# Kernel tuning notes

Hardware: AMD Instinct MI355X
Metric: run time of the kernel (lower is better)

## Reference

```python
import jax, jax.numpy as jnp
import numpy as np

N_NODES = 50000
N_EDGES = 400000
D_NODE = 256
D_EDGE = 64
HEADS = 32          # node_hidden_size // 8
HEAD_DIM = 8        # node_hidden_size // heads
LRELU = 0.01


def _lin_init(key, fan_in, fan_out, bias=True):
    kw, kb = jax.random.split(key)
    s = 1.0 / np.sqrt(fan_in)
    W = jax.random.uniform(kw, (fan_in, fan_out), jnp.float32, -s, s)
    if bias:
        b = jax.random.uniform(kb, (fan_out,), jnp.float32, -s, s)
        return W, b
    return W


def setup_inputs() -> dict:
    key = jax.random.key(0)
    ks = jax.random.split(key, 12)
    x = jax.random.normal(ks[0], (N_NODES, D_NODE), jnp.float32)
    edge_index = jax.random.randint(ks[1], (2, N_EDGES), 0, N_NODES, jnp.int64)
    edge_attr = jax.random.normal(ks[2], (N_EDGES, D_EDGE), jnp.float32)
    Wq, bq = _lin_init(ks[3], D_NODE, D_NODE)
    Wk, bk = _lin_init(ks[4], D_NODE, D_NODE)
    Wv, bv = _lin_init(ks[5], D_NODE, D_NODE)
    We = _lin_init(ks[6], D_EDGE, D_NODE, bias=False)   # lin_edge has no bias in PyG
    Ws, bs = _lin_init(ks[7], D_NODE, D_NODE)           # root/skip connection
    W1, b1 = _lin_init(ks[8], 2 * D_NODE + D_EDGE, D_EDGE)
    W2, b2 = _lin_init(ks[9], D_EDGE, D_EDGE)
    return dict(x=x, edge_index=edge_index, edge_attr=edge_attr,
                Wq=Wq, bq=bq, Wk=Wk, bk=bk, Wv=Wv, bv=bv, We=We,
                Ws=Ws, bs=bs, W1=W1, b1=b1, W2=W2, b2=b2)


def _leaky(v, alpha=LRELU):
    return jnp.where(v >= 0, v, alpha * v)


def reference(x, edge_index, edge_attr, Wq, bq, Wk, bk, Wv, bv, We, Ws, bs, W1, b1, W2, b2):
    N = x.shape[0]
    src, dst = edge_index[0], edge_index[1]

    # ---- TransformerConv (concat heads, root weight, edge_dim) ----
    q = (x @ Wq + bq).reshape(N, HEADS, HEAD_DIM)
    k = (x @ Wk + bk).reshape(N, HEADS, HEAD_DIM)
    v = (x @ Wv + bv).reshape(N, HEADS, HEAD_DIM)
    e = (edge_attr @ We).reshape(-1, HEADS, HEAD_DIM)           # [E,H,C]

    k_j = k[src] + e                                            # [E,H,C]
    alpha = jnp.einsum('ehc,ehc->eh', q[dst], k_j) / np.sqrt(HEAD_DIM)
    # segment softmax over destination nodes
    amax = jax.ops.segment_max(alpha, dst, num_segments=N)      # [N,H]
    ex = jnp.exp(alpha - amax[dst])
    denom = jax.ops.segment_sum(ex, dst, num_segments=N)        # [N,H]
    attn = ex / (denom[dst] + 1e-16)                            # [E,H]

    msg = (v[src] + e) * attn[:, :, None]                       # [E,H,C]
    out = jax.ops.segment_sum(msg, dst, num_segments=N).reshape(N, D_NODE)
    out = out + (x @ Ws + bs)                                   # skip / root weight

    x_new = _leaky(out)                                         # block activation

    # ---- EdgeResidualLayer ----
    h = jnp.concatenate([x_new[src], x_new[dst], edge_attr], axis=-1)  # [E,576]
    h = _leaky(h @ W1 + b1)
    edge_new = edge_attr + (h @ W2 + b2)
    edge_new = _leaky(edge_new)

    return (x_new, edge_new)
```

## Files before the change

### kernel.cpp

```cpp
#include <hip/hip_runtime.h>
#include <hip/hip_bf16.h>


#define N_NODES 50000
#define N_EDGES 400000
#define D_NODE 256
#define D_EDGE 64
#define HEADS 32
#define LRELU 0.01f
#define SEG 16

typedef __hip_bfloat16 bf16;
typedef __attribute__((ext_vector_type(8))) short short8b;
typedef __attribute__((ext_vector_type(4))) float f32x4;
typedef __attribute__((ext_vector_type(4))) unsigned short ushort4v;
typedef __attribute__((ext_vector_type(4))) int int4v;

__device__ __forceinline__ float bf2f(bf16 v) { return __bfloat162float(v); }
__device__ __forceinline__ bf16 f2bf(float f) { return __float2bfloat16(f); }
__device__ __forceinline__ float bfraw(unsigned short u) {
    return __uint_as_float(((unsigned int)u) << 16);
}
__device__ __forceinline__ unsigned short rawbf(float f) {
    bf16 t = f2bf(f); return *(unsigned short*)&t;
}
__device__ __forceinline__ float leaky(float v) { return v >= 0.f ? v : LRELU * v; }
__device__ __forceinline__ short8b pack8(const f32x4 a, const f32x4 b) {
    short8b r;
    r[0] = (short)rawbf(a[0]); r[1] = (short)rawbf(a[1]);
    r[2] = (short)rawbf(a[2]); r[3] = (short)rawbf(a[3]);
    r[4] = (short)rawbf(b[0]); r[5] = (short)rawbf(b[1]);
    r[6] = (short)rawbf(b[2]); r[7] = (short)rawbf(b[3]);
    return r;
}

__global__ void k0_detect(const int* __restrict__ ei, int* __restrict__ flags)
{
    const int lane = threadIdx.x;
    const unsigned long long mz = __ballot(ei[2 * lane + 1] == 0);
    if (lane == 0) flags[0] = (__popcll(mz) >= 48) ? 1 : 0;
}

__device__ __forceinline__ void load_edge(const int* ei, int f, int i, int& s, int& d)
{
    if (f) {
        const long long* e64 = (const long long*)ei;
        s = (int)e64[i]; d = (int)e64[N_EDGES + i];
    } else {
        s = ei[i]; d = ei[N_EDGES + i];
    }
}

__global__ __launch_bounds__(256) void kcd_degree(
    const int* __restrict__ ei, const int* __restrict__ flags, int* __restrict__ deg)
{
    const int i = blockIdx.x * 256 + threadIdx.x;
    if (i >= N_EDGES) return;
    int s, d; load_edge(ei, flags[0], i, s, d);
    atomicAdd(&deg[d], 1);
}

__global__ __launch_bounds__(1024) void kcs_scan(int* __restrict__ cur)
{
    __shared__ int ps[1024];
    const int t = threadIdx.x;
    const int CHN = (N_NODES + 1023) / 1024;
    const int base = t * CHN;
    int sum = 0;
    for (int i = 0; i < CHN; ++i) {
        const int n = base + i;
        if (n < N_NODES) sum += cur[n];
    }
    ps[t] = sum;
    __syncthreads();
    for (int off = 1; off < 1024; off <<= 1) {
        const int v = (t >= off) ? ps[t - off] : 0;
        __syncthreads();
        ps[t] += v;
        __syncthreads();
    }
    int excl = (t == 0) ? 0 : ps[t - 1];
    for (int i = 0; i < CHN; ++i) {
        const int n = base + i;
        if (n < N_NODES) {
            const int d = cur[n];
            cur[n] = excl;
            excl += d;
        }
    }
}

__global__ __launch_bounds__(256) void kct_scatter(
    const int* __restrict__ ei, const int* __restrict__ flags, int* __restrict__ cursor,
    int* __restrict__ ssort, int* __restrict__ dsort, int* __restrict__ eidsort)
{
    const int i = blockIdx.x * 256 + threadIdx.x;
    if (i >= N_EDGES) return;
    int s, d; load_edge(ei, flags[0], i, s, d);
    const int pos = atomicAdd(&cursor[d], 1);
    ssort[pos] = s; dsort[pos] = d; eidsort[pos] = i;
}

__global__ __launch_bounds__(256) void kT_transpose(
    const float* __restrict__ We, const float* __restrict__ W1, const float* __restrict__ W2,
    const float* __restrict__ Wq, const float* __restrict__ Wk,
    const float* __restrict__ Wv, const float* __restrict__ Ws,
    bf16* __restrict__ WeTf, bf16* __restrict__ W1sdf, bf16* __restrict__ W1eaf,
    bf16* __restrict__ W2Tf, bf16* __restrict__ WT4f)
{
    const int gid = blockIdx.x * 256 + threadIdx.x;
    const int gsz = gridDim.x * 256;
    for (int i = gid; i < 4 * 16 * 8 * 512; i += gsz) {
        const int j = i & 7, l = (i >> 3) & 63, kc = (i >> 9) & 7;
        const int ct = (i >> 12) & 15, m = i >> 16;
        const int row = l & 15, kg = l >> 4;
        const int n = ct * 16 + row, k = kc * 32 + kg * 8 + j;
        const float* W = (m == 0) ? Wq : (m == 1) ? Wk : (m == 2) ? Wv : Ws;
        WT4f[i] = f2bf(W[k * 256 + n]);
    }
    for (int i = gid; i < 16 * 2 * 512; i += gsz) {
        const int j = i & 7, l = (i >> 3) & 63, kc = (i >> 9) & 1, ct = i >> 10;
        const int row = l & 15, kg = l >> 4;
        const int n = ct * 16 + row, k = kc * 32 + kg * 8 + j;
        WeTf[i] = f2bf(We[k * 256 + n]);
    }
    for (int i = gid; i < 2 * 4 * 8 * 512; i += gsz) {
        const int j = i & 7, l = (i >> 3) & 63, kc = (i >> 9) & 7;
        const int ct = (i >> 12) & 3, m2 = i >> 14;
        const int row = l & 15, kg = l >> 4;
        const int n = ct * 16 + row;
        const int k = m2 * 256 + kc * 32 + kg * 8 + j;
        W1sdf[i] = f2bf(W1[k * 64 + n]);
    }
    for (int i = gid; i < 4 * 2 * 512; i += gsz) {
        const int j = i & 7, l = (i >> 3) & 63, kc = (i >> 9) & 1, ct = i >> 10;
        const int row = l & 15, kg = l >> 4;
        const int n = ct * 16 + row;
        const int k = 512 + kc * 32 + kg * 8 + j;
        W1eaf[i] = f2bf(W1[k * 64 + n]);
    }
    for (int i = gid; i < 4 * 2 * 512; i += gsz) {
        const int j = i & 7, l = (i >> 3) & 63, kc = (i >> 9) & 1, ct = i >> 10;
        const int row = l & 15, kg = l >> 4;
        const int n = ct * 16 + row, k = kc * 32 + kg * 8 + j;
        W2Tf[i] = f2bf(W2[k * 64 + n]);
    }
}

#define X_LD 264
__global__ __launch_bounds__(256) void k1_node_mfma(
    const float* __restrict__ x, const bf16* __restrict__ WT4f,
    const float* __restrict__ bq, const float* __restrict__ bk,
    const float* __restrict__ bv, const float* __restrict__ bs,
    bf16* __restrict__ qo, bf16* __restrict__ kvb,
    bf16* __restrict__ skipb)
{
    __shared__ unsigned short xs[64 * X_LD];
    const int tid = threadIdx.x;
    const int n0 = blockIdx.x * 64;
    const int w = tid >> 6, l = tid & 63;
    const int row = l & 15, kg = l >> 4;

    {
        const int e = tid >> 2, t = tid & 3;
        const int nmine = n0 + e;
        const f32x4* src = (const f32x4*)(x + (size_t)nmine * 256 + t * 64);
        #pragma unroll
        for (int c = 0; c < 4; ++c) {
            unsigned short tmp[16];
            if (nmine < N_NODES) {
                #pragma unroll
                for (int u = 0; u < 4; ++u) {
                    const f32x4 v = __builtin_nontemporal_load(src + c * 4 + u);
                    tmp[u * 4 + 0] = rawbf(v[0]); tmp[u * 4 + 1] = rawbf(v[1]);
                    tmp[u * 4 + 2] = rawbf(v[2]); tmp[u * 4 + 3] = rawbf(v[3]);
                }
            } else {
                #pragma unroll
                for (int u = 0; u < 16; ++u) tmp[u] = 0;
            }
            *(short8b*)&xs[e * X_LD + t * 64 + c * 16]     = *(short8b*)&tmp[0];
            *(short8b*)&xs[e * X_LD + t * 64 + c * 16 + 8] = *(short8b*)&tmp[8];
        }
    }
    short8b af[8];
    #pragma unroll
    for (int kc = 0; kc < 8; ++kc)
        af[kc] = *(const short8b*)&xs[(w * 16 + row) * X_LD + kc * 32 + kg * 8];

    for (int m = 0; m < 4; ++m) {
        const float* bias = (m == 0) ? bq : (m == 1) ? bk : (m == 2) ? bv : bs;
        #pragma unroll 4
        for (int ct = 0; ct < 16; ++ct) {
            const float bvv = bias[ct * 16 + row];
            f32x4 acc = {bvv, bvv, bvv, bvv};
            #pragma unroll
            for (int kc = 0; kc < 8; ++kc) {
                const short8b bfr = *(const short8b*)(WT4f + (((size_t)((m * 16 + ct) * 8 + kc)) << 9) + l * 8);
                acc = __builtin_amdgcn_mfma_f32_16x16x32_bf16(af[kc], bfr, acc, 0, 0, 0);
            }
            #pragma unroll
            for (int r = 0; r < 4; ++r)
                xs[(w * 16 + kg * 4 + r) * X_LD + ct * 16 + row] = rawbf(acc[r]);
        }
        {
            #pragma unroll
            for (int u = 0; u < 8; ++u) {
                const int flat = u * 64 + l;
                const int node = w * 16 + (flat >> 5);
                const int col8 = (flat & 31) * 8;
                if (n0 + node < N_NODES) {
                    const short8b vdat = *(const short8b*)&xs[node * X_LD + col8];
                    bf16* dp;
                    if (m == 0)      dp = qo    + (size_t)(n0 + node) * 256 + col8;
                    else if (m == 1) dp = kvb   + (size_t)(n0 + node) * 512 + col8;
                    else if (m == 2) dp = kvb   + (size_t)(n0 + node) * 512 + 256 + col8;
                    else             dp = skipb + (size_t)(n0 + node) * 256 + col8;
                    *(short8b*)dp = vdat;
                }
            }
        }
    }
}

#define EP_LD 264
__global__ __launch_bounds__(256) void k2_seg(
    const int* __restrict__ ssort, const int* __restrict__ dsort,
    const int* __restrict__ eidsort, const int* __restrict__ endptr,
    const float* __restrict__ ea, const bf16* __restrict__ WeTf,
    const bf16* __restrict__ q, const bf16* __restrict__ kvb,
    const bf16* __restrict__ skipb, const bf16* __restrict__ W1sdf,
    float* __restrict__ out_x, bf16* __restrict__ xnb, bf16* __restrict__ P)
{
    __shared__ float acc_s[SEG * 256];
    __shared__ float den_s[SEG * HEADS];
    __shared__ unsigned short ep_s[64 * EP_LD];
    const int tid = threadIdx.x;
    const int n0 = blockIdx.x * SEG;

    #pragma unroll
    for (int i = 0; i < SEG; ++i) acc_s[i * 256 + tid] = 0.f;
    if (tid < SEG * HEADS - 256) den_s[256 + tid] = 0.f;
    den_s[tid] = 0.f;

    const int start = (n0 == 0) ? 0 : endptr[n0 - 1];
    const int end   = endptr[n0 + SEG - 1];
    __syncthreads();

    const int w = tid >> 6, l = tid & 63;
    const int row = l & 15, kg = l >> 4;
    const float scale = 0.35355339059327373f;

    for (int sbase = start + w * 16; sbase < end; sbase += 64) {
        const int cnt = min(16, end - sbase);

        short8b af0 = {0, 0, 0, 0, 0, 0, 0, 0}, af1 = af0;
        if (row < cnt) {
            const int eg = eidsort[sbase + row];
            const float* pb = ea + (size_t)eg * 64 + kg * 8;
            const f32x4 a0 = __builtin_nontemporal_load((const f32x4*)pb);
            const f32x4 a1 = __builtin_nontemporal_load((const f32x4*)(pb + 4));
            const f32x4 b0 = __builtin_nontemporal_load((const f32x4*)(pb + 32));
            const f32x4 b1 = __builtin_nontemporal_load((const f32x4*)(pb + 36));
            af0 = pack8(a0, a1); af1 = pack8(b0, b1);
        }

        int sv = 0;
        if (l < 16)      { if (l < cnt)      sv = ssort[sbase + l]; }
        else if (l < 32) { if (l - 16 < cnt) sv = dsort[sbase + (l - 16)]; }

        ushort4v kvv[16], vvv[16];
        #pragma unroll
        for (int i = 0; i < 16; ++i) {
            const int s = __shfl(sv, min(i, cnt - 1));
            const bf16* base = kvb + (size_t)s * 512;
            kvv[i] = *(const ushort4v*)(base + l * 4);
            vvv[i] = *(const ushort4v*)(base + 256 + l * 4);
        }
        __builtin_amdgcn_sched_barrier(0);

        #pragma unroll 4
        for (int ct = 0; ct < 16; ++ct) {
            f32x4 acc = {0.f, 0.f, 0.f, 0.f};
            const short8b b0 = *(const short8b*)(WeTf + (ct * 2 + 0) * 512 + l * 8);
            const short8b b1 = *(const short8b*)(WeTf + (ct * 2 + 1) * 512 + l * 8);
            acc = __builtin_amdgcn_mfma_f32_16x16x32_bf16(af0, b0, acc, 0, 0, 0);
            acc = __builtin_amdgcn_mfma_f32_16x16x32_bf16(af1, b1, acc, 0, 0, 0);
            #pragma unroll
            for (int r = 0; r < 4; ++r)
                ep_s[(w * 16 + kg * 4 + r) * EP_LD + ct * 16 + row] = rawbf(acc[r]);
        }

        float macc[4] = {0.f, 0.f, 0.f, 0.f};
        float dacc = 0.f;
        int dprev = -1;
        ushort4v qv = {0, 0, 0, 0};

        #pragma unroll
        for (int i = 0; i < 16; ++i) {
            const int d = __shfl(sv, 16 + min(i, cnt - 1));
            if (d != dprev) {
                if (dprev >= 0) {
                    const int ld = dprev - n0;
                    #pragma unroll
                    for (int t = 0; t < 4; ++t)
                        atomicAdd(&acc_s[ld * 256 + l * 4 + t], macc[t]);
                    if ((l & 1) == 0)
                        atomicAdd(&den_s[ld * HEADS + (l >> 1)], dacc);
                    macc[0] = macc[1] = macc[2] = macc[3] = 0.f;
                    dacc = 0.f;
                }
                qv = *(const ushort4v*)(q + (size_t)d * 256 + l * 4);
                dprev = d;
            }
            const ushort4v ep = *(const ushort4v*)&ep_s[(w * 16 + i) * EP_LD + l * 4];
            float p = 0.f, m4[4];
            #pragma unroll
            for (int t = 0; t < 4; ++t) {
                const float epf = bfraw(ep[t]);
                p = fmaf(bfraw(qv[t]), bfraw(kvv[i][t]) + epf, p);
                m4[t] = bfraw(vvv[i][t]) + epf;
            }
            p += __shfl_xor(p, 1);
            const float ex = (i < cnt) ? __expf(p * scale) : 0.f;
            #pragma unroll
            for (int t = 0; t < 4; ++t) macc[t] = fmaf(m4[t], ex, macc[t]);
            dacc += ex;
        }
        {
            const int ld = dprev - n0;
            #pragma unroll
            for (int t = 0; t < 4; ++t)
                atomicAdd(&acc_s[ld * 256 + l * 4 + t], macc[t]);
            if ((l & 1) == 0)
                atomicAdd(&den_s[ld * HEADS + (l >> 1)], dacc);
        }
    }
    __syncthreads();

    #pragma unroll
    for (int u = 0; u < 4; ++u) {
        const int flat4 = u * 256 + tid;
        const int node = flat4 >> 6;
        const int ch4 = flat4 & 63;
        const int n = n0 + node;
        const float den = den_s[node * HEADS + (ch4 >> 1)] + 1e-16f;
        const f32x4 mv = *(const f32x4*)&acc_s[node * 256 + ch4 * 4];
        const ushort4v sk = *(const ushort4v*)(skipb + (size_t)n * 256 + ch4 * 4);
        f32x4 o; ushort4v ob;
        #pragma unroll
        for (int t = 0; t < 4; ++t) {
            const float xn = leaky(mv[t] / den + bfraw(sk[t]));
            o[t] = xn; ob[t] = rawbf(xn);
        }
        *(f32x4*)(out_x + (size_t)n * 256 + ch4 * 4) = o;
        *(ushort4v*)(xnb + (size_t)n * 256 + ch4 * 4) = ob;
        *(ushort4v*)&ep_s[node * EP_LD + ch4 * 4] = ob;
    }
    __syncthreads();

    {
        short8b af2[8];
        #pragma unroll
        for (int kc = 0; kc < 8; ++kc)
            af2[kc] = *(const short8b*)&ep_s[row * EP_LD + kc * 32 + kg * 8];
        #pragma unroll
        for (int c2 = 0; c2 < 2; ++c2) {
            const int ct = w * 2 + c2;
            const int m2 = ct >> 2, ct4 = ct & 3;
            f32x4 acc = {0.f, 0.f, 0.f, 0.f};
            #pragma unroll
            for (int kc = 0; kc < 8; ++kc) {
                const short8b bfr = *(const short8b*)(W1sdf + ((m2 * 4 + ct4) * 8 + kc) * 512 + l * 8);
                acc = __builtin_amdgcn_mfma_f32_16x16x32_bf16(af2[kc], bfr, acc, 0, 0, 0);
            }
            #pragma unroll
            for (int r = 0; r < 4; ++r)
                P[(size_t)(n0 + kg * 4 + r) * 128 + m2 * 64 + row * 4 + ct4] = f2bf(acc[r]);
        }
    }
}

__global__ __launch_bounds__(256) void k4_edge_mlp(
    const int* __restrict__ ssort, const int* __restrict__ dsort,
    const int* __restrict__ eidsort,
    const bf16* __restrict__ P, const float* __restrict__ ea,
    const bf16* __restrict__ W1eaf, const float* __restrict__ b1,
    const bf16* __restrict__ W2Tf, const float* __restrict__ b2,
    float* __restrict__ out_e)
{
    __shared__ unsigned short h2_s[4][16 * 72];
    __shared__ unsigned short ea_s[4][16 * 72];
    const int tid = threadIdx.x;
    const int w = tid >> 6, l = tid & 63;
    const int row = l & 15, kg = l >> 4;

    const int q8 = (N_EDGES / 64) >> 3, r8 = (N_EDGES / 64) & 7;
    const int xcd = blockIdx.x & 7, idx = blockIdx.x >> 3;
    const int bid = (xcd < r8 ? xcd * (q8 + 1) : r8 * (q8 + 1) + (xcd - r8) * q8) + idx;
    const int e0 = bid * 64;
    const int sl = e0 + w * 16 + row;
    const int eg = eidsort[sl];

    const int cr0 = e0 + w * 16 + kg * 4;
    const int4v s4  = *(const int4v*)(ssort + cr0);
    const int4v d4  = *(const int4v*)(dsort + cr0);
    const int4v eg4 = *(const int4v*)(eidsort + cr0);

    const float* pb = ea + (size_t)eg * 64 + kg * 8;
    const f32x4 a0 = __builtin_nontemporal_load((const f32x4*)pb);
    const f32x4 a1 = __builtin_nontemporal_load((const f32x4*)(pb + 4));
    const f32x4 c0 = __builtin_nontemporal_load((const f32x4*)(pb + 32));
    const f32x4 c1 = __builtin_nontemporal_load((const f32x4*)(pb + 36));

    const unsigned short* Pu = (const unsigned short*)P;
    ushort4v ps4[4], pd4[4];
    #pragma unroll
    for (int r = 0; r < 4; ++r) {
        ps4[r] = *(const ushort4v*)(Pu + (size_t)s4[r] * 128 + row * 4);
        pd4[r] = *(const ushort4v*)(Pu + (size_t)d4[r] * 128 + 64 + row * 4);
    }
    __builtin_amdgcn_sched_barrier(0);

    const short8b afr0 = pack8(a0, a1);
    const short8b afr1 = pack8(c0, c1);
    *(short8b*)&ea_s[w][row * 72 + kg * 8]      = afr0;
    *(short8b*)&ea_s[w][row * 72 + 32 + kg * 8] = afr1;

    f32x4 acc[4];
    #pragma unroll
    for (int ct = 0; ct < 4; ++ct) {
        const float bvv = b1[ct * 16 + row];
        acc[ct] = (f32x4){bvv, bvv, bvv, bvv};
    }
    #pragma unroll
    for (int kc = 0; kc < 2; ++kc) {
        const short8b af = (kc == 0) ? afr0 : afr1;
        #pragma unroll
        for (int ct = 0; ct < 4; ++ct) {
            const short8b bfr = *(const short8b*)(W1eaf + (ct * 2 + kc) * 512 + l * 8);
            acc[ct] = __builtin_amdgcn_mfma_f32_16x16x32_bf16(af, bfr, acc[ct], 0, 0, 0);
        }
    }
    #pragma unroll
    for (int ct = 0; ct < 4; ++ct)
        #pragma unroll
        for (int r = 0; r < 4; ++r)
            acc[ct][r] += bfraw(ps4[r][ct]) + bfraw(pd4[r][ct]);

    unsigned short* h2 = h2_s[w];
    #pragma unroll
    for (int ct = 0; ct < 4; ++ct)
        #pragma unroll
        for (int r = 0; r < 4; ++r)
            h2[(kg * 4 + r) * 72 + ct * 16 + row] = rawbf(leaky(acc[ct][r]));

    f32x4 a2[4];
    #pragma unroll
    for (int ct = 0; ct < 4; ++ct) {
        const float bvv = b2[ct * 16 + row];
        a2[ct] = (f32x4){bvv, bvv, bvv, bvv};
    }
    #pragma unroll
    for (int kc = 0; kc < 2; ++kc) {
        const short8b af = *(const short8b*)&h2[row * 72 + kc * 32 + kg * 8];
        #pragma unroll
        for (int ct = 0; ct < 4; ++ct) {
            const short8b bfr = *(const short8b*)(W2Tf + (ct * 2 + kc) * 512 + l * 8);
            a2[ct] = __builtin_amdgcn_mfma_f32_16x16x32_bf16(af, bfr, a2[ct], 0, 0, 0);
        }
    }

    #pragma unroll
    for (int ct = 0; ct < 4; ++ct)
        #pragma unroll
        for (int r = 0; r < 4; ++r) {
            const float eav = bfraw(ea_s[w][(kg * 4 + r) * 72 + ct * 16 + row]);
            out_e[(size_t)eg4[r] * 64 + ct * 16 + row] = leaky(eav + a2[ct][r]);
        }
}

extern "C" void kernel_launch(void* const* d_in, const int* in_sizes, int n_in,
                              void* d_out, int out_size, void* d_ws, size_t ws_size,
                              hipStream_t stream)
{
    const float* x  = (const float*)d_in[0];
    const int*   ei = (const int*)d_in[1];
    const float* ea = (const float*)d_in[2];
    const float* Wq = (const float*)d_in[3];
    const float* bq = (const float*)d_in[4];
    const float* Wk = (const float*)d_in[5];
    const float* bk = (const float*)d_in[6];
    const float* Wv = (const float*)d_in[7];
    const float* bv = (const float*)d_in[8];
    const float* We = (const float*)d_in[9];
    const float* Ws = (const float*)d_in[10];
    const float* bs = (const float*)d_in[11];
    const float* W1 = (const float*)d_in[12];
    const float* b1 = (const float*)d_in[13];
    const float* W2 = (const float*)d_in[14];
    const float* b2 = (const float*)d_in[15];

    char* ws = (char*)d_ws;
    int*   flags  = (int*)ws;
    int*   ssort  = (int*)(ws + 4096);
    int*   dsort  = (int*)(ws + 1604096);
    int*   eids   = (int*)(ws + 3204096);
    int*   cursor = (int*)(ws + 4804096);
    bf16*  WeTf   = (bf16*)(ws + 5004096);
    bf16*  W1sdf  = (bf16*)(ws + 5036864);
    bf16*  W1eaf  = (bf16*)(ws + 5102400);
    bf16*  W2Tf   = (bf16*)(ws + 5110592);
    bf16*  WT4f   = (bf16*)(ws + 5118784);
    bf16*  qb     = (bf16*)(ws + 5643072);
    bf16*  kvb    = (bf16*)(ws + 31243072);
    bf16*  xnb    = (bf16*)(ws + 82443072);
    bf16*  Pp     = (bf16*)(ws + 108100000);

    float* out_x = (float*)d_out;
    float* out_e = out_x + (size_t)N_NODES * D_NODE;
    bf16*  skipb = (bf16*)out_e;

    hipMemsetAsync(cursor, 0, N_NODES * 4, stream);

    k0_detect<<<1, 64, 0, stream>>>(ei, flags);
    kcd_degree<<<(N_EDGES + 255) / 256, 256, 0, stream>>>(ei, flags, cursor);
    kcs_scan<<<1, 1024, 0, stream>>>(cursor);
    kct_scatter<<<(N_EDGES + 255) / 256, 256, 0, stream>>>(ei, flags, cursor, ssort, dsort, eids);

    kT_transpose<<<64, 256, 0, stream>>>(We, W1, W2, Wq, Wk, Wv, Ws,
                                         WeTf, W1sdf, W1eaf, W2Tf, WT4f);

    k1_node_mfma<<<(N_NODES + 63) / 64, 256, 0, stream>>>(
        x, WT4f, bq, bk, bv, bs, qb, kvb, skipb);

    k2_seg<<<N_NODES / SEG, 256, 0, stream>>>(
        ssort, dsort, eids, cursor, ea, WeTf, qb, kvb, skipb, W1sdf,
        out_x, xnb, Pp);

    k4_edge_mlp<<<N_EDGES / 64, 256, 0, stream>>>(
        ssort, dsort, eids, Pp, ea, W1eaf, b1, W2Tf, b2, out_e);
}
```

Before: 561.9 us.

## Pre-permute edge attributes to sorted bf16 buffer and drop unused xnb store

Adds a kernel that gathers edge_attr in destination-sorted order and converts it to a contiguous bf16 buffer. The segment and edge-MLP kernels then read half-size, coalesced rows instead of doing random fp32 gathers through eidsort, and the edge-MLP no longer stages edge attributes in shared memory. The unused bf16 x_new write is also removed. The cost is one extra pass that reads ea (fp32, random) and writes a 51MB bf16 copy, plus an extra launch.

```diff
diff --git a/kernel.cpp b/kernel.cpp
--- a/kernel.cpp
+++ b/kernel.cpp
@@ -99,6 +99,26 @@
     int s, d; load_edge(ei, flags[0], i, s, d);
     const int pos = atomicAdd(&cursor[d], 1);
     ssort[pos] = s; dsort[pos] = d; eidsort[pos] = i;
+}
+
+__global__ __launch_bounds__(256) void keir_reorder(
+    const int* __restrict__ eidsort, const float* __restrict__ ea,
+    bf16* __restrict__ easb)
+{
+    const int tid = threadIdx.x;
+    const int e = blockIdx.x * 64 + (tid >> 2);
+    const int t = tid & 3;
+    const int eg = eidsort[e];
+    const f32x4* src = (const f32x4*)(ea + (size_t)eg * 64 + t * 16);
+    unsigned short tmp[16];
+    #pragma unroll
+    for (int u = 0; u < 4; ++u) {
+        const f32x4 v = __builtin_nontemporal_load(src + u);
+        tmp[u * 4 + 0] = rawbf(v[0]); tmp[u * 4 + 1] = rawbf(v[1]);
+        tmp[u * 4 + 2] = rawbf(v[2]); tmp[u * 4 + 3] = rawbf(v[3]);
+    }
+    *(short8b*)(easb + (size_t)e * 64 + t * 16)     = *(short8b*)&tmp[0];
+    *(short8b*)(easb + (size_t)e * 64 + t * 16 + 8) = *(short8b*)&tmp[8];
 }
 
 __global__ __launch_bounds__(256) void kT_transpose(
@@ -226,11 +246,11 @@
 #define EP_LD 264
 __global__ __launch_bounds__(256) void k2_seg(
     const int* __restrict__ ssort, const int* __restrict__ dsort,
-    const int* __restrict__ eidsort, const int* __restrict__ endptr,
-    const float* __restrict__ ea, const bf16* __restrict__ WeTf,
+    const int* __restrict__ endptr,
+    const bf16* __restrict__ easb, const bf16* __restrict__ WeTf,
     const bf16* __restrict__ q, const bf16* __restrict__ kvb,
     const bf16* __restrict__ skipb, const bf16* __restrict__ W1sdf,
-    float* __restrict__ out_x, bf16* __restrict__ xnb, bf16* __restrict__ P)
+    float* __restrict__ out_x, bf16* __restrict__ P)
 {
     __shared__ float acc_s[SEG * 256];
     __shared__ float den_s[SEG * HEADS];
@@ -256,13 +276,9 @@
 
         short8b af0 = {0, 0, 0, 0, 0, 0, 0, 0}, af1 = af0;
         if (row < cnt) {
-            const int eg = eidsort[sbase + row];
-            const float* pb = ea + (size_t)eg * 64 + kg * 8;
-            const f32x4 a0 = __builtin_nontemporal_load((const f32x4*)pb);
-            const f32x4 a1 = __builtin_nontemporal_load((const f32x4*)(pb + 4));
-            const f32x4 b0 = __builtin_nontemporal_load((const f32x4*)(pb + 32));
-            const f32x4 b1 = __builtin_nontemporal_load((const f32x4*)(pb + 36));
-            af0 = pack8(a0, a1); af1 = pack8(b0, b1);
+            const bf16* pe = easb + (size_t)(sbase + row) * 64;
+            af0 = *(const short8b*)(pe + kg * 8);
+            af1 = *(const short8b*)(pe + 32 + kg * 8);
         }
 
         int sv = 0;
@@ -354,7 +370,6 @@
             o[t] = xn; ob[t] = rawbf(xn);
         }
         *(f32x4*)(out_x + (size_t)n * 256 + ch4 * 4) = o;
-        *(ushort4v*)(xnb + (size_t)n * 256 + ch4 * 4) = ob;
         *(ushort4v*)&ep_s[node * EP_LD + ch4 * 4] = ob;
     }
     __syncthreads();
@@ -384,13 +399,12 @@
 __global__ __launch_bounds__(256) void k4_edge_mlp(
     const int* __restrict__ ssort, const int* __restrict__ dsort,
     const int* __restrict__ eidsort,
-    const bf16* __restrict__ P, const float* __restrict__ ea,
+    const bf16* __restrict__ P, const bf16* __restrict__ easb,
     const bf16* __restrict__ W1eaf, const float* __restrict__ b1,
     const bf16* __restrict__ W2Tf, const float* __restrict__ b2,
     float* __restrict__ out_e)
 {
     __shared__ unsigned short h2_s[4][16 * 72];
-    __shared__ unsigned short ea_s[4][16 * 72];
     const int tid = threadIdx.x;
     const int w = tid >> 6, l = tid & 63;
     const int row = l & 15, kg = l >> 4;
@@ -400,18 +414,15 @@
     const int bid = (xcd < r8 ? xcd * (q8 + 1) : r8 * (q8 + 1) + (xcd - r8) * q8) + idx;
     const int e0 = bid * 64;
     const int sl = e0 + w * 16 + row;
-    const int eg = eidsort[sl];
 
     const int cr0 = e0 + w * 16 + kg * 4;
     const int4v s4  = *(const int4v*)(ssort + cr0);
     const int4v d4  = *(const int4v*)(dsort + cr0);
     const int4v eg4 = *(const int4v*)(eidsort + cr0);
 
-    const float* pb = ea + (size_t)eg * 64 + kg * 8;
-    const f32x4 a0 = __builtin_nontemporal_load((const f32x4*)pb);
-    const f32x4 a1 = __builtin_nontemporal_load((const f32x4*)(pb + 4));
-    const f32x4 c0 = __builtin_nontemporal_load((const f32x4*)(pb + 32));
-    const f32x4 c1 = __builtin_nontemporal_load((const f32x4*)(pb + 36));
+    const bf16* pe = easb + (size_t)sl * 64;
+    const short8b afr0 = *(const short8b*)(pe + kg * 8);
+    const short8b afr1 = *(const short8b*)(pe + 32 + kg * 8);
 
     const unsigned short* Pu = (const unsigned short*)P;
     ushort4v ps4[4], pd4[4];
@@ -422,11 +433,6 @@
     }
     __builtin_amdgcn_sched_barrier(0);
 
-    const short8b afr0 = pack8(a0, a1);
-    const short8b afr1 = pack8(c0, c1);
-    *(short8b*)&ea_s[w][row * 72 + kg * 8]      = afr0;
-    *(short8b*)&ea_s[w][row * 72 + 32 + kg * 8] = afr1;
-
     f32x4 acc[4];
     #pragma unroll
     for (int ct = 0; ct < 4; ++ct) {
@@ -475,7 +481,7 @@
     for (int ct = 0; ct < 4; ++ct)
         #pragma unroll
         for (int r = 0; r < 4; ++r) {
-            const float eav = bfraw(ea_s[w][(kg * 4 + r) * 72 + ct * 16 + row]);
+            const float eav = bfraw(*(const unsigned short*)(easb + (size_t)(cr0 + r) * 64 + ct * 16 + row));
             out_e[(size_t)eg4[r] * 64 + ct * 16 + row] = leaky(eav + a2[ct][r]);
         }
 }
@@ -514,8 +520,8 @@
     bf16*  WT4f   = (bf16*)(ws + 5118784);
     bf16*  qb     = (bf16*)(ws + 5643072);
     bf16*  kvb    = (bf16*)(ws + 31243072);
-    bf16*  xnb    = (bf16*)(ws + 82443072);
-    bf16*  Pp     = (bf16*)(ws + 108100000);
+    bf16*  easb   = (bf16*)(ws + 82443072);
+    bf16*  Pp     = (bf16*)(ws + 133643072);
 
     float* out_x = (float*)d_out;
     float* out_e = out_x + (size_t)N_NODES * D_NODE;
@@ -531,13 +537,15 @@
     kT_transpose<<<64, 256, 0, stream>>>(We, W1, W2, Wq, Wk, Wv, Ws,
                                          WeTf, W1sdf, W1eaf, W2Tf, WT4f);
 
+    keir_reorder<<<N_EDGES / 64, 256, 0, stream>>>(eids, ea, easb);
+
     k1_node_mfma<<<(N_NODES + 63) / 64, 256, 0, stream>>>(
         x, WT4f, bq, bk, bv, bs, qb, kvb, skipb);
 
     k2_seg<<<N_NODES / SEG, 256, 0, stream>>>(
-        ssort, dsort, eids, cursor, ea, WeTf, qb, kvb, skipb, W1sdf,
-        out_x, xnb, Pp);
+        ssort, dsort, cursor, easb, WeTf, qb, kvb, skipb, W1sdf,
+        out_x, Pp);
 
     k4_edge_mlp<<<N_EDGES / 64, 256, 0, stream>>>(
-        ssort, dsort, eids, Pp, ea, W1eaf, b1, W2Tf, b2, out_e);
-}
+        ssort, dsort, eids, Pp, easb, W1eaf, b1, W2Tf, b2, out_e);
+}
```

Result: no change. 566.4 us (+0.8%).
